# Kernel optimization log

Hardware: AMD Instinct MI355X
Metric: run time of the kernel (lower is better)

Reference implementation:

```python
import jax, jax.numpy as jnp
import numpy as np

N = 50000       # nodes
E = 800000      # edges (avg degree 16)
D_IN = 128      # input_dim
H = 256         # hidden_dim
Z = H // 2      # 128, latent / conv3-4 width
D_OUT = 64      # output_dim


def _glorot(key, shape):
    fan_in, fan_out = shape
    lim = float(np.sqrt(6.0 / (fan_in + fan_out)))
    return jax.random.uniform(key, shape, jnp.float32, -lim, lim)


def setup_inputs() -> dict:
    key = jax.random.key(0)
    ks = jax.random.split(key, 16)
    inp = {
        "x": jax.random.uniform(ks[0], (N, D_IN), jnp.float32),
        "edge_index": jax.random.randint(ks[1], (2, E), 0, N, jnp.int32),
        "epsilon": jax.random.normal(ks[2], (N, Z), jnp.float32),
        # SAGEConv params: Wl (neighbor/aggr path, with bias), Wr (root path, no bias)
        "Wl1": _glorot(ks[3], (D_IN, H)), "bl1": jnp.zeros((H,), jnp.float32), "Wr1": _glorot(ks[4], (D_IN, H)),
        "Wl2": _glorot(ks[5], (H, H)),    "bl2": jnp.zeros((H,), jnp.float32), "Wr2": _glorot(ks[6], (H, H)),
        "Wl3": _glorot(ks[7], (Z, Z)),    "bl3": jnp.zeros((Z,), jnp.float32), "Wr3": _glorot(ks[8], (Z, Z)),
        "Wl4": _glorot(ks[9], (Z, Z)),    "bl4": jnp.zeros((Z,), jnp.float32), "Wr4": _glorot(ks[10], (Z, Z)),
        "W_lin": _glorot(ks[11], (Z, D_OUT)), "b_lin": jnp.zeros((D_OUT,), jnp.float32),
    }
    return inp


def _sage_conv(x, src, dst, Wl, bl, Wr):
    # PyG SAGEConv (mean aggr): out = lin_l(mean_{j in N(i)} x_j) + lin_r(x_i)
    msg = x[src]                                             # [E, d] gather
    agg = jax.ops.segment_sum(msg, dst, num_segments=N)      # [N, d]
    cnt = jax.ops.segment_sum(jnp.ones((src.shape[0],), x.dtype), dst, num_segments=N)
    mean = agg / jnp.maximum(cnt, 1.0)[:, None]
    return mean @ Wl + bl + x @ Wr


def reference(x, edge_index, epsilon,
              Wl1, bl1, Wr1, Wl2, bl2, Wr2,
              Wl3, bl3, Wr3, Wl4, bl4, Wr4,
              W_lin, b_lin):
    src, dst = edge_index[0], edge_index[1]
    h = x / 1000.0 - 0.5
    h = jnp.sin(_sage_conv(h, src, dst, Wl1, bl1, Wr1))      # [N, H]
    h = _sage_conv(h, src, dst, Wl2, bl2, Wr2)               # [N, H]
    mean = h[:, :Z]
    log_var = h[:, Z:]
    z = mean + jnp.exp(log_var) * epsilon                    # reparameterize
    h = jax.nn.relu(_sage_conv(z, src, dst, Wl3, bl3, Wr3))
    h = jax.nn.relu(_sage_conv(h, src, dst, Wl4, bl4, Wr4))
    out = jax.nn.sigmoid(h @ W_lin + b_lin) * 1000.0
    return out, mean, log_var
```

## Files before the change

kernel.cpp:

```cpp
#include <hip/hip_runtime.h>
#include <hip/hip_bf16.h>

#define N_NODES 50000
#define E_EDGES 800000

using u16 = unsigned short;
typedef short bf8 __attribute__((ext_vector_type(8)));
typedef float f32x4 __attribute__((ext_vector_type(4)));

__device__ __forceinline__ float bf2f(u16 h) {
    union { unsigned u; float f; } v;
    v.u = ((unsigned)h) << 16;
    return v.f;
}
__device__ __forceinline__ u16 f2bf(float f) {
    union { float f; unsigned u; } v;
    v.f = f;
    unsigned r = v.u + 0x7FFF + ((v.u >> 16) & 1);
    return (u16)(r >> 16);
}

#define GLOAD_LDS16(gsrc, ldst)                                            \
    __builtin_amdgcn_global_load_lds(                                      \
        (const __attribute__((address_space(1))) void*)(gsrc),             \
        (__attribute__((address_space(3))) void*)(ldst), 16, 0, 0)

struct WtArgs {
    const float* src[9];
    u16* dst[9];
    int K[9];
    int N[9];
};

__global__ __launch_bounds__(256) void k_wpack(WtArgs a) {
    int wi = blockIdx.y;
    int K = a.K[wi], NC = a.N[wi];
    int KS = K / 32;
    int chunks = (NC / 16) * KS * 64;
    for (int c = blockIdx.x * 256 + threadIdx.x; c < chunks;
         c += gridDim.x * 256) {
        int l = c & 63;
        int rest = c >> 6;
        int ks = rest % KS, gni = rest / KS;
        int n = gni * 16 + (l & 15);
        int kb = ks * 32 + (l >> 4) * 8;
        u16 outv[8];
#pragma unroll
        for (int j = 0; j < 8; ++j)
            outv[j] = f2bf(a.src[wi][(size_t)(kb + j) * NC + n]);
        *(bf8*)&a.dst[wi][(size_t)c * 8] = *(bf8*)outv;
    }
}

__global__ __launch_bounds__(256) void k_prep(const float* __restrict__ x,
                                              u16* __restrict__ h0) {
    int total = N_NODES * 128 / 4;
    for (int i = blockIdx.x * 256 + threadIdx.x; i < total;
         i += gridDim.x * 256) {
        float4 v = *(const float4*)(x + (size_t)i * 4);
        ushort4 o;
        o.x = f2bf(v.x * 0.001f - 0.5f);
        o.y = f2bf(v.y * 0.001f - 0.5f);
        o.z = f2bf(v.z * 0.001f - 0.5f);
        o.w = f2bf(v.w * 0.001f - 0.5f);
        *(ushort4*)(h0 + (size_t)i * 4) = o;
    }
}

__global__ void k_count(const int* __restrict__ dst, int* __restrict__ deg,
                        int* __restrict__ rank) {
    for (int i = blockIdx.x * blockDim.x + threadIdx.x; i < E_EDGES;
         i += gridDim.x * blockDim.x)
        rank[i] = atomicAdd(&deg[dst[i]], 1);
}

#define SCAN_B 49

__global__ __launch_bounds__(1024) void k_scan1(const int* __restrict__ deg,
                                                int* __restrict__ bsum) {
    __shared__ int sm[1024];
    int i = blockIdx.x * 1024 + threadIdx.x;
    sm[threadIdx.x] = (i < N_NODES) ? deg[i] : 0;
    __syncthreads();
    for (int ofs = 512; ofs > 0; ofs >>= 1) {
        if (threadIdx.x < ofs) sm[threadIdx.x] += sm[threadIdx.x + ofs];
        __syncthreads();
    }
    if (threadIdx.x == 0) bsum[blockIdx.x] = sm[0];
}

__global__ void k_scan2(const int* __restrict__ bsum, int* __restrict__ bofs) {
    int l = threadIdx.x;
    int v = (l < SCAN_B) ? bsum[l] : 0;
    int orig = v;
    for (int d = 1; d < 64; d <<= 1) {
        int u = __shfl_up(v, d, 64);
        if (l >= d) v += u;
    }
    if (l < SCAN_B) bofs[l] = v - orig;
}

__global__ __launch_bounds__(1024) void k_scan3(const int* __restrict__ deg,
                                                const int* __restrict__ bofs,
                                                int* __restrict__ rowptr,
                                                float* __restrict__ dinv) {
    __shared__ int sm[1024];
    int i = blockIdx.x * 1024 + threadIdx.x;
    int d = (i < N_NODES) ? deg[i] : 0;
    sm[threadIdx.x] = d;
    __syncthreads();
    for (int ofs = 1; ofs < 1024; ofs <<= 1) {
        int u = (threadIdx.x >= (unsigned)ofs) ? sm[threadIdx.x - ofs] : 0;
        __syncthreads();
        sm[threadIdx.x] += u;
        __syncthreads();
    }
    if (i < N_NODES) {
        int incl = sm[threadIdx.x] + bofs[blockIdx.x];
        rowptr[i] = incl - d;
        dinv[i] = 1.0f / fmaxf((float)d, 1.0f);
        if (i == N_NODES - 1) rowptr[N_NODES] = incl;
    }
}

__global__ void k_fill(const int* __restrict__ src, const int* __restrict__ dst,
                       const int* __restrict__ rowptr,
                       const int* __restrict__ rank,
                       int* __restrict__ colidx) {
    for (int i = blockIdx.x * blockDim.x + threadIdx.x; i < E_EDGES;
         i += gridDim.x * blockDim.x) {
        int d = dst[i];
        colidx[rowptr[d] + rank[i]] = src[i];
    }
}

template <int D>
__global__ __launch_bounds__(256) void k_aggregate(
    const u16* __restrict__ h, const int* __restrict__ rowptr,
    const int* __restrict__ colidx, const float* __restrict__ dinv,
    u16* __restrict__ mean) {
    constexpr int VA = D / 16;
    int node = (int)((blockIdx.x * 256 + threadIdx.x) >> 6);
    int lane = threadIdx.x & 63;
    if (node >= N_NODES) return;
    int sub = lane >> 4, lr = lane & 15;
    int beg = rowptr[node], end = rowptr[node + 1];
    int deg = end - beg;
    float acc[VA] = {};
    for (int base = 0; base < deg; base += 64) {
        int nb = min(64, deg - base);
        int idx = 0;
        if (lane < nb) idx = colidx[beg + base + lane];
        int j = 0;
        for (; j + 8 <= nb; j += 8) {
            int s0 = __shfl(idx, j + sub, 64);
            int s1 = __shfl(idx, j + 4 + sub, 64);
            const u16* p0 = h + (size_t)s0 * D + lr * VA;
            const u16* p1 = h + (size_t)s1 * D + lr * VA;
            bf8 r0 = *(const bf8*)p0;
            bf8 r1 = *(const bf8*)p1;
            if (VA == 16) {
                bf8 r0b = *(const bf8*)(p0 + 8);
                bf8 r1b = *(const bf8*)(p1 + 8);
#pragma unroll
                for (int q = 0; q < 8; ++q) {
                    acc[q] += bf2f((u16)r0[q]) + bf2f((u16)r1[q]);
                    acc[8 + q] += bf2f((u16)r0b[q]) + bf2f((u16)r1b[q]);
                }
            } else {
#pragma unroll
                for (int q = 0; q < 8; ++q)
                    acc[q] += bf2f((u16)r0[q]) + bf2f((u16)r1[q]);
            }
        }
        for (; j < nb; j += 4) {
            int e = j + sub;
            int ec = min(e, nb - 1);
            int s = __shfl(idx, ec, 64);
            if (e < nb) {
                const u16* row = h + (size_t)s * D + lr * VA;
                bf8 r0 = *(const bf8*)row;
#pragma unroll
                for (int q = 0; q < 8; ++q) acc[q] += bf2f((u16)r0[q]);
                if (VA == 16) {
                    bf8 r1 = *(const bf8*)(row + 8);
#pragma unroll
                    for (int q = 0; q < 8; ++q) acc[8 + q] += bf2f((u16)r1[q]);
                }
            }
        }
    }
#pragma unroll
    for (int j = 0; j < VA; ++j) {
        acc[j] += __shfl_xor(acc[j], 16);
        acc[j] += __shfl_xor(acc[j], 32);
    }
    if (sub == 0) {
        float inv = dinv[node];
        u16 outv[VA];
#pragma unroll
        for (int j = 0; j < VA; ++j) outv[j] = f2bf(acc[j] * inv);
        u16* o = mean + (size_t)node * D + lr * VA;
        *(bf8*)o = *(bf8*)&outv[0];
        if (VA == 16) *(bf8*)(o + 8) = *(bf8*)&outv[8];
    }
}

enum { ACT_NONE = 0, ACT_SIN = 1, ACT_RELU = 2, ACT_SIGMOID1000 = 3, ACT_VAE = 4 };

template <int K, int NCB, int NC, int YS, int ACT, bool OUT_F32, bool TWO_PASS>
__global__ __launch_bounds__(512) void k_gemm(
    const u16* __restrict__ A1, const u16* __restrict__ Wp1,
    const u16* __restrict__ A2, const u16* __restrict__ Wp2,
    const float* __restrict__ bias, void* __restrict__ Cout,
    float* __restrict__ out_mean, float* __restrict__ out_lv,
    const float* __restrict__ eps) {
    constexpr int M = N_NODES;
    constexpr int NG = NCB / 16;
    constexpr int KS1 = K / 32;
    constexpr int KST = TWO_PASS ? 2 * KS1 : KS1;
    constexpr int CH1 = NG * KS1 * 64;
    constexpr int GX = (M / 16 + 7) / 8;
    constexpr int NWG = ((GX * YS + 7) / 8) * 8;
    constexpr int CPX = NWG / 8;
    extern __shared__ char smem[];
    u16* Bs = (u16*)smem;

    const int bid = blockIdx.x;
    const int wid = (bid & 7) * CPX + (bid >> 3);
    const int x = wid / YS;
    const int y = wid % YS;
    if (x >= GX) return;

    const int t = threadIdx.x;
    const int lane = t & 63;
    const int wave = t >> 6;
    const int lr = lane & 15;
    const int sub = lane >> 4;
    const int row0 = (x * 8 + wave) * 16;
    const int arow = row0 + lr;
    const bool rowOK = arow < M;

    auto mapGroup = [&](int ni) {
        if (ACT == ACT_VAE)
            return ni < NG / 2 ? y * (NG / 2) + ni
                               : (NC / 32) + y * (NG / 2) + (ni - NG / 2);
        return y * NG + ni;
    };

    {
#pragma unroll
        for (int i = 0; i < CH1 / 512; ++i) {
            int c = t + i * 512;
            int ks = (c >> 6) % KS1;
            int ni = c / (64 * KS1);
            const u16* gsrc =
                Wp1 + (((size_t)mapGroup(ni) * KS1 + ks) * 64 + lane) * 8;
            u16* ldst = Bs + ((size_t)(i * 512 + wave * 64)) * 8;
            GLOAD_LDS16(gsrc, ldst);
        }
        if (TWO_PASS) {
#pragma unroll
            for (int i = 0; i < CH1 / 512; ++i) {
                int c = t + i * 512;
                int ks = (c >> 6) % KS1;
                int ni = c / (64 * KS1);
                const u16* gsrc =
                    Wp2 + (((size_t)mapGroup(ni) * KS1 + ks) * 64 + lane) * 8;
                u16* ldst = Bs + ((size_t)(CH1 + i * 512 + wave * 64)) * 8;
                GLOAD_LDS16(gsrc, ldst);
            }
        }
    }

    float epsv[ACT == ACT_VAE ? 8 : 1];
    if (ACT == ACT_VAE) {
#pragma unroll
        for (int ni = 0; ni < NG / 2; ++ni) {
#pragma unroll
            for (int r = 0; r < 4; ++r) {
                int row = row0 + sub * 4 + r;
                int colm = y * (NCB / 2) + ni * 16 + lr;
                epsv[ni * 4 + r] =
                    (row < M) ? eps[(size_t)row * 128 + colm] : 0.f;
            }
        }
    }

    f32x4 acc[NG];
#pragma unroll
    for (int i = 0; i < NG; ++i) acc[i] = (f32x4){0.f, 0.f, 0.f, 0.f};

    auto aptr = [&](int ks) {
        return (ks < KS1 ? A1 + (size_t)arow * K + ks * 32
                         : A2 + (size_t)arow * K + (ks - KS1) * 32) +
               sub * 8;
    };

    __syncthreads();

    bf8 acur = {0, 0, 0, 0, 0, 0, 0, 0};
    if (rowOK) acur = *(const bf8*)aptr(0);
#pragma unroll
    for (int ks = 0; ks < KST; ++ks) {
        bf8 anext = {0, 0, 0, 0, 0, 0, 0, 0};
        if (ks + 1 < KST && rowOK) anext = *(const bf8*)aptr(ks + 1);
#pragma unroll
        for (int ni = 0; ni < NG; ++ni) {
            size_t off = (ks < KS1)
                             ? (((size_t)ni * KS1 + ks) * 64)
                             : ((size_t)CH1 +
                                ((size_t)ni * KS1 + (ks - KS1)) * 64);
            bf8 b = *(const bf8*)&Bs[(off + lane) * 8];
            acc[ni] =
                __builtin_amdgcn_mfma_f32_16x16x32_bf16(acur, b, acc[ni], 0, 0, 0);
        }
        acur = anext;
    }

    if (ACT == ACT_VAE) {
#pragma unroll
        for (int ni = 0; ni < NG / 2; ++ni) {
            int colm = y * (NCB / 2) + ni * 16 + lr;
            float bm = bias[colm];
            float bl = bias[colm + 128];
#pragma unroll
            for (int r = 0; r < 4; ++r) {
                int row = row0 + sub * 4 + r;
                if (row >= M) continue;
                float mv = acc[ni][r] + bm;
                float lv = acc[ni + NG / 2][r] + bl;
                size_t o = (size_t)row * 128 + colm;
                out_mean[o] = mv;
                out_lv[o] = lv;
                ((u16*)Cout)[o] = f2bf(mv + __expf(lv) * epsv[ni * 4 + r]);
            }
        }
    } else {
#pragma unroll
        for (int ni = 0; ni < NG; ++ni) {
            int col = y * NCB + ni * 16 + lr;
            float bv = bias[col];
#pragma unroll
            for (int r = 0; r < 4; ++r) {
                int row = row0 + sub * 4 + r;
                if (row >= M) continue;
                float v = acc[ni][r] + bv;
                if (ACT == ACT_SIN) v = __sinf(v);
                else if (ACT == ACT_RELU) v = fmaxf(v, 0.f);
                else if (ACT == ACT_SIGMOID1000) v = 1000.f / (1.f + __expf(-v));
                if (OUT_F32)
                    ((float*)Cout)[(size_t)row * NC + col] = v;
                else
                    ((u16*)Cout)[(size_t)row * NC + col] = f2bf(v);
            }
        }
    }
}

extern "C" void kernel_launch(void* const* d_in, const int* in_sizes, int n_in,
                              void* d_out, int out_size, void* d_ws,
                              size_t ws_size, hipStream_t stream) {
    const int N = N_NODES;
    const float* x = (const float*)d_in[0];
    const int* ei = (const int*)d_in[1];
    const float* eps = (const float*)d_in[2];
    const float* Wl1 = (const float*)d_in[3];
    const float* bl1 = (const float*)d_in[4];
    const float* Wr1 = (const float*)d_in[5];
    const float* Wl2 = (const float*)d_in[6];
    const float* bl2 = (const float*)d_in[7];
    const float* Wr2 = (const float*)d_in[8];
    const float* Wl3 = (const float*)d_in[9];
    const float* bl3 = (const float*)d_in[10];
    const float* Wr3 = (const float*)d_in[11];
    const float* Wl4 = (const float*)d_in[12];
    const float* bl4 = (const float*)d_in[13];
    const float* Wr4 = (const float*)d_in[14];
    const float* W_lin = (const float*)d_in[15];
    const float* b_lin = (const float*)d_in[16];

    const int* src = ei;
    const int* dst = ei + E_EDGES;

    char* w = (char*)d_ws;
    auto alloc = [&](size_t b) {
        void* p = (void*)w;
        w += (b + 255) & ~(size_t)255;
        return p;
    };
    int* deg = (int*)alloc((size_t)N * 4);
    int* rowptr = (int*)alloc((size_t)(N + 1) * 4);
    int* rank = (int*)alloc((size_t)E_EDGES * 4);
    int* colidx = (int*)alloc((size_t)E_EDGES * 4);
    float* dinv = (float*)alloc((size_t)N * 4);
    int* bsum = (int*)alloc(64 * 4);
    int* bofs = (int*)alloc(64 * 4);
    u16* hbA = (u16*)alloc((size_t)N * 256 * 2);
    u16* hbB = (u16*)alloc((size_t)N * 256 * 2);
    u16* hbC = (u16*)alloc((size_t)N * 256 * 2);
    static const int wK[9] = {128, 128, 256, 256, 128, 128, 128, 128, 128};
    static const int wN[9] = {256, 256, 256, 256, 128, 128, 128, 128, 64};
    u16* Wt[9];
    for (int i = 0; i < 9; ++i) Wt[i] = (u16*)alloc((size_t)wK[i] * wN[i] * 2);

    float* out_final = (float*)d_out;
    float* out_mean = out_final + (size_t)N * 64;
    float* out_lv = out_mean + (size_t)N * 128;

    hipMemsetAsync(deg, 0, (size_t)N * 4, stream);

    WtArgs wa;
    const float* wsrc[9] = {Wl1, Wr1, Wl2, Wr2, Wl3, Wr3, Wl4, Wr4, W_lin};
    for (int i = 0; i < 9; ++i) {
        wa.src[i] = wsrc[i];
        wa.dst[i] = Wt[i];
        wa.K[i] = wK[i];
        wa.N[i] = wN[i];
    }
    k_wpack<<<dim3(32, 9), 256, 0, stream>>>(wa);

    k_prep<<<2048, 256, 0, stream>>>(x, hbA);
    k_count<<<3125, 256, 0, stream>>>(dst, deg, rank);
    k_scan1<<<SCAN_B, 1024, 0, stream>>>(deg, bsum);
    k_scan2<<<1, 64, 0, stream>>>(bsum, bofs);
    k_scan3<<<SCAN_B, 1024, 0, stream>>>(deg, bofs, rowptr, dinv);
    k_fill<<<3125, 256, 0, stream>>>(src, dst, rowptr, rank, colidx);

    const int aggBlocks = (N * 64 + 255) / 256;
    auto nwg = [](int YS) { return ((391 * YS + 7) / 8) * 8; };
    auto shm = [](int NCB, int Ktot) { return (size_t)NCB * Ktot * 2; };

    k_aggregate<128><<<aggBlocks, 256, 0, stream>>>(hbA, rowptr, colidx, dinv,
                                                    hbB);
    k_gemm<128, 64, 256, 4, ACT_SIN, false, true>
        <<<nwg(4), 512, shm(64, 256), stream>>>(hbB, Wt[0], hbA, Wt[1], bl1,
                                                hbC, nullptr, nullptr, nullptr);

    k_aggregate<256><<<aggBlocks, 256, 0, stream>>>(hbC, rowptr, colidx, dinv,
                                                    hbB);
    k_gemm<256, 64, 256, 4, ACT_VAE, false, true>
        <<<nwg(4), 512, shm(64, 512), stream>>>(hbB, Wt[2], hbC, Wt[3], bl2,
                                                hbA, out_mean, out_lv, eps);

    k_aggregate<128><<<aggBlocks, 256, 0, stream>>>(hbA, rowptr, colidx, dinv,
                                                    hbB);
    k_gemm<128, 64, 128, 2, ACT_RELU, false, true>
        <<<nwg(2), 512, shm(64, 256), stream>>>(hbB, Wt[4], hbA, Wt[5], bl3,
                                                hbC, nullptr, nullptr, nullptr);

    k_aggregate<128><<<aggBlocks, 256, 0, stream>>>(hbC, rowptr, colidx, dinv,
                                                    hbB);
    k_gemm<128, 64, 128, 2, ACT_RELU, false, true>
        <<<nwg(2), 512, shm(64, 256), stream>>>(hbB, Wt[6], hbC, Wt[7], bl4,
                                                hbA, nullptr, nullptr, nullptr);

    k_gemm<128, 32, 64, 2, ACT_SIGMOID1000, true, false>
        <<<nwg(2), 512, shm(32, 128), stream>>>(hbA, Wt[8], nullptr, nullptr,
                                                b_lin, out_final, nullptr,
                                                nullptr, nullptr);
}
```

Before: 318.6 us.

## Split aggregation across feature slices so each wave gathers 16 edges at once

Rewrites the mean-aggregation kernel so each block handles one 32-wide feature slice for four nodes. Within a wave, each lane loads 16 bytes (8 bf16) and 16 neighbor rows are fetched concurrently. The goal is more memory-level parallelism per wave and a higher share of the gathered row landing in cache. In exchange, the grid is 4-8x larger, colidx and rowptr are re-read once per slice, and the final reduction needs two extra shuffle stages.

```diff
diff --git a/kernel.cpp b/kernel.cpp
--- a/kernel.cpp
+++ b/kernel.cpp
@@ -139,70 +139,51 @@
     const u16* __restrict__ h, const int* __restrict__ rowptr,
     const int* __restrict__ colidx, const float* __restrict__ dinv,
     u16* __restrict__ mean) {
-    constexpr int VA = D / 16;
-    int node = (int)((blockIdx.x * 256 + threadIdx.x) >> 6);
-    int lane = threadIdx.x & 63;
+    constexpr int SLICES = D / 32;
+    const int slice = blockIdx.x % SLICES;
+    const int node = (blockIdx.x / SLICES) * 4 + (threadIdx.x >> 6);
+    const int lane = threadIdx.x & 63;
     if (node >= N_NODES) return;
-    int sub = lane >> 4, lr = lane & 15;
+    const int sub4 = lane >> 2, lr4 = lane & 3;
+    const u16* hs = h + slice * 32 + lr4 * 8;
     int beg = rowptr[node], end = rowptr[node + 1];
     int deg = end - beg;
-    float acc[VA] = {};
+    float acc[8] = {};
     for (int base = 0; base < deg; base += 64) {
         int nb = min(64, deg - base);
         int idx = 0;
         if (lane < nb) idx = colidx[beg + base + lane];
         int j = 0;
-        for (; j + 8 <= nb; j += 8) {
-            int s0 = __shfl(idx, j + sub, 64);
-            int s1 = __shfl(idx, j + 4 + sub, 64);
-            const u16* p0 = h + (size_t)s0 * D + lr * VA;
-            const u16* p1 = h + (size_t)s1 * D + lr * VA;
-            bf8 r0 = *(const bf8*)p0;
-            bf8 r1 = *(const bf8*)p1;
-            if (VA == 16) {
-                bf8 r0b = *(const bf8*)(p0 + 8);
-                bf8 r1b = *(const bf8*)(p1 + 8);
-#pragma unroll
-                for (int q = 0; q < 8; ++q) {
-                    acc[q] += bf2f((u16)r0[q]) + bf2f((u16)r1[q]);
-                    acc[8 + q] += bf2f((u16)r0b[q]) + bf2f((u16)r1b[q]);
-                }
-            } else {
-#pragma unroll
-                for (int q = 0; q < 8; ++q)
-                    acc[q] += bf2f((u16)r0[q]) + bf2f((u16)r1[q]);
-            }
-        }
-        for (; j < nb; j += 4) {
-            int e = j + sub;
+        for (; j + 16 <= nb; j += 16) {
+            int s = __shfl(idx, j + sub4, 64);
+            bf8 r = *(const bf8*)(hs + (size_t)s * D);
+#pragma unroll
+            for (int q = 0; q < 8; ++q) acc[q] += bf2f((u16)r[q]);
+        }
+        if (j < nb) {
+            int e = j + sub4;
             int ec = min(e, nb - 1);
             int s = __shfl(idx, ec, 64);
             if (e < nb) {
-                const u16* row = h + (size_t)s * D + lr * VA;
-                bf8 r0 = *(const bf8*)row;
-#pragma unroll
-                for (int q = 0; q < 8; ++q) acc[q] += bf2f((u16)r0[q]);
-                if (VA == 16) {
-                    bf8 r1 = *(const bf8*)(row + 8);
-#pragma unroll
-                    for (int q = 0; q < 8; ++q) acc[8 + q] += bf2f((u16)r1[q]);
-                }
+                bf8 r = *(const bf8*)(hs + (size_t)s * D);
+#pragma unroll
+                for (int q = 0; q < 8; ++q) acc[q] += bf2f((u16)r[q]);
             }
         }
     }
 #pragma unroll
-    for (int j = 0; j < VA; ++j) {
-        acc[j] += __shfl_xor(acc[j], 16);
-        acc[j] += __shfl_xor(acc[j], 32);
-    }
-    if (sub == 0) {
+    for (int q = 0; q < 8; ++q) {
+        acc[q] += __shfl_xor(acc[q], 4);
+        acc[q] += __shfl_xor(acc[q], 8);
+        acc[q] += __shfl_xor(acc[q], 16);
+        acc[q] += __shfl_xor(acc[q], 32);
+    }
+    if (sub4 == 0) {
         float inv = dinv[node];
-        u16 outv[VA];
-#pragma unroll
-        for (int j = 0; j < VA; ++j) outv[j] = f2bf(acc[j] * inv);
-        u16* o = mean + (size_t)node * D + lr * VA;
-        *(bf8*)o = *(bf8*)&outv[0];
-        if (VA == 16) *(bf8*)(o + 8) = *(bf8*)&outv[8];
+        u16 outv[8];
+#pragma unroll
+        for (int q = 0; q < 8; ++q) outv[q] = f2bf(acc[q] * inv);
+        *(bf8*)(mean + (size_t)node * D + slice * 32 + lr4 * 8) = *(bf8*)outv;
     }
 }
 
@@ -427,30 +408,30 @@
     k_scan3<<<SCAN_B, 1024, 0, stream>>>(deg, bofs, rowptr, dinv);
     k_fill<<<3125, 256, 0, stream>>>(src, dst, rowptr, rank, colidx);
 
-    const int aggBlocks = (N * 64 + 255) / 256;
+    const int nodeGroups = (N + 3) / 4;
     auto nwg = [](int YS) { return ((391 * YS + 7) / 8) * 8; };
     auto shm = [](int NCB, int Ktot) { return (size_t)NCB * Ktot * 2; };
 
-    k_aggregate<128><<<aggBlocks, 256, 0, stream>>>(hbA, rowptr, colidx, dinv,
-                                                    hbB);
+    k_aggregate<128><<<nodeGroups * 4, 256, 0, stream>>>(hbA, rowptr, colidx,
+                                                         dinv, hbB);
     k_gemm<128, 64, 256, 4, ACT_SIN, false, true>
         <<<nwg(4), 512, shm(64, 256), stream>>>(hbB, Wt[0], hbA, Wt[1], bl1,
                                                 hbC, nullptr, nullptr, nullptr);
 
-    k_aggregate<256><<<aggBlocks, 256, 0, stream>>>(hbC, rowptr, colidx, dinv,
-                                                    hbB);
+    k_aggregate<256><<<nodeGroups * 8, 256, 0, stream>>>(hbC, rowptr, colidx,
+                                                         dinv, hbB);
     k_gemm<256, 64, 256, 4, ACT_VAE, false, true>
         <<<nwg(4), 512, shm(64, 512), stream>>>(hbB, Wt[2], hbC, Wt[3], bl2,
                                                 hbA, out_mean, out_lv, eps);
 
-    k_aggregate<128><<<aggBlocks, 256, 0, stream>>>(hbA, rowptr, colidx, dinv,
-                                                    hbB);
+    k_aggregate<128><<<nodeGroups * 4, 256, 0, stream>>>(hbA, rowptr, colidx,
+                                                         dinv, hbB);
     k_gemm<128, 64, 128, 2, ACT_RELU, false, true>
         <<<nwg(2), 512, shm(64, 256), stream>>>(hbB, Wt[4], hbA, Wt[5], bl3,
                                                 hbC, nullptr, nullptr, nullptr);
 
-    k_aggregate<128><<<aggBlocks, 256, 0, stream>>>(hbC, rowptr, colidx, dinv,
-                                                    hbB);
+    k_aggregate<128><<<nodeGroups * 4, 256, 0, stream>>>(hbC, rowptr, colidx,
+                                                         dinv, hbB);
     k_gemm<128, 64, 128, 2, ACT_RELU, false, true>
         <<<nwg(2), 512, shm(64, 256), stream>>>(hbB, Wt[6], hbC, Wt[7], bl4,
                                                 hbA, nullptr, nullptr, nullptr);
```

Result: slower. 546.4 us (+71.5%).
